# Kernel tuning notes

Measured on AMD Instinct MI355X. Metric: run time of the kernel, lower is better.

Reference implementation:

```python
import jax, jax.numpy as jnp
import numpy as np

T, B, D = 200, 1024, 128
T_OBS = 140
L = 20       # rec_dims: encoder latent per mean/std
LAT = 32     # latents: generative latent dim
GRU_U = 200  # gru_units
UNITS = 100  # hidden units of ODE-func / z0 nets


def _lin(key, fan_in, fan_out):
    return jax.random.normal(key, (fan_in, fan_out), jnp.float32) / jnp.sqrt(jnp.float32(fan_in))


def setup_inputs() -> dict:
    key = jax.random.key(0)
    ks = jax.random.split(key, 20)
    gin = 2 * L + 2 * D  # GRU input: (mean,std) + (data,mask)
    inp = {
        "truth": jax.random.normal(ks[0], (T, B, D), jnp.float32),
        "t": jnp.arange(T, dtype=jnp.float32),
        "obs_idx": jnp.sort(jax.random.randint(ks[1], (T_OBS,), 0, T)),
        "eps": jax.random.normal(ks[2], (B, LAT), jnp.float32),
        # encoder ODE func (rec_layers=1 hidden layer of UNITS)
        "enc_w1": _lin(ks[3], L, UNITS), "enc_b1": jnp.zeros(UNITS, jnp.float32),
        "enc_w2": _lin(ks[4], UNITS, L), "enc_b2": jnp.zeros(L, jnp.float32),
        # GRU unit: update / reset / new-state nets
        "gru_uw1": _lin(ks[5], gin, GRU_U), "gru_ub1": jnp.zeros(GRU_U, jnp.float32),
        "gru_uw2": _lin(ks[6], GRU_U, 2 * L), "gru_ub2": jnp.zeros(2 * L, jnp.float32),
        "gru_rw1": _lin(ks[7], gin, GRU_U), "gru_rb1": jnp.zeros(GRU_U, jnp.float32),
        "gru_rw2": _lin(ks[8], GRU_U, 2 * L), "gru_rb2": jnp.zeros(2 * L, jnp.float32),
        "gru_nw1": _lin(ks[9], gin, GRU_U), "gru_nb1": jnp.zeros(GRU_U, jnp.float32),
        "gru_nw2": _lin(ks[10], GRU_U, 2 * L), "gru_nb2": jnp.zeros(2 * L, jnp.float32),
        # transform hidden -> z0 (mean,std)
        "z0_w1": _lin(ks[11], 2 * L, UNITS), "z0_b1": jnp.zeros(UNITS, jnp.float32),
        "z0_w2": _lin(ks[12], UNITS, 2 * LAT), "z0_b2": jnp.zeros(2 * LAT, jnp.float32),
        # decoder ODE func (gen_layers=2 hidden layers of UNITS)
        "dec_w1": _lin(ks[13], LAT, UNITS), "dec_b1": jnp.zeros(UNITS, jnp.float32),
        "dec_w2": _lin(ks[14], UNITS, UNITS), "dec_b2": jnp.zeros(UNITS, jnp.float32),
        "dec_w3": _lin(ks[15], UNITS, LAT), "dec_b3": jnp.zeros(LAT, jnp.float32),
        # readout latent -> data space
        "out_w": _lin(ks[16], LAT, D), "out_b": jnp.zeros(D, jnp.float32),
    }
    return inp


def _rk4(f, y, dt):
    k1 = f(y)
    k2 = f(y + 0.5 * dt * k1)
    k3 = f(y + 0.5 * dt * k2)
    k4 = f(y + dt * k3)
    return y + (dt / 6.0) * (k1 + 2.0 * k2 + 2.0 * k3 + k4)


def reference(truth, t, obs_idx, eps,
              enc_w1, enc_b1, enc_w2, enc_b2,
              gru_uw1, gru_ub1, gru_uw2, gru_ub2,
              gru_rw1, gru_rb1, gru_rw2, gru_rb2,
              gru_nw1, gru_nb1, gru_nw2, gru_nb2,
              z0_w1, z0_b1, z0_w2, z0_b2,
              dec_w1, dec_b1, dec_w2, dec_b2, dec_w3, dec_b3,
              out_w, out_b):
    enc_f = lambda y: jnp.tanh(y @ enc_w1 + enc_b1) @ enc_w2 + enc_b2
    dec_f = lambda z: (jnp.tanh(jnp.tanh(z @ dec_w1 + dec_b1) @ dec_w2 + dec_b2)
                       @ dec_w3 + dec_b3)

    # ----- ODE-RNN encoder, run_backwards=True over observed timesteps -----
    x_obs = truth[obs_idx][::-1]                     # [To, B, D], time-reversed
    t_obs = t[obs_idx][::-1]
    dts = jnp.concatenate([jnp.zeros(1, t.dtype), jnp.diff(t_obs)])  # <=0 steps

    def enc_step(carry, inp):
        ym, ys = carry                               # [B,L] each
        x, dt = inp
        ym = _rk4(enc_f, ym, dt)                     # evolve mean between obs
        xm = jnp.concatenate([x, jnp.ones_like(x)], -1)   # data + mask(=1)
        y = jnp.concatenate([ym, ys], -1)            # [B, 2L]
        yc = jnp.concatenate([y, xm], -1)            # [B, 2L+2D]
        u = jax.nn.sigmoid(jnp.tanh(yc @ gru_uw1 + gru_ub1) @ gru_uw2 + gru_ub2)
        r = jax.nn.sigmoid(jnp.tanh(yc @ gru_rw1 + gru_rb1) @ gru_rw2 + gru_rb2)
        nc = jnp.concatenate([y * r, xm], -1)
        ns = jnp.tanh(nc @ gru_nw1 + gru_nb1) @ gru_nw2 + gru_nb2
        nm, nsd = ns[:, :L], jnp.abs(ns[:, L:])
        new_y = (1.0 - u) * jnp.concatenate([nm, nsd], -1) + u * y
        return (new_y[:, :L], new_y[:, L:]), None

    nb = truth.shape[1]
    init = (jnp.zeros((nb, L), truth.dtype), jnp.zeros((nb, L), truth.dtype))
    (ym, ys), _ = jax.lax.scan(enc_step, init, (x_obs, dts))

    # ----- z0 posterior and sample (n_traj_samples=1) -----
    h = jnp.tanh(jnp.concatenate([ym, ys], -1) @ z0_w1 + z0_b1) @ z0_w2 + z0_b2
    z0_mean, z0_std = h[:, :LAT], jnp.abs(h[:, LAT:])
    z = z0_mean + eps * z0_std                       # [B, LAT]

    # ----- Neural ODE decoder over time_steps_to_predict = t -----
    def dec_step(zc, dt):
        zn = _rk4(dec_f, zc, dt)
        return zn, zn
    _, zs = jax.lax.scan(dec_step, z, jnp.diff(t))
    sol = jnp.concatenate([z[None], zs], 0)          # [T, B, LAT]

    out = sol @ out_w + out_b                        # [T, B, D]
    return jnp.transpose(out, (1, 0, 2))[None]       # [1, B, T, D]
```

## Files before the change

kernel.cpp:

```cpp
#include <hip/hip_runtime.h>
#include <math.h>

#define BB 1024
#define DD 128
#define NWG 256
#define CH 28
#define NCH 5

#define WS_WPACK 0
#define WS_B1E   81920
#define WS_W1Y   82560
#define WS_Y     106560
#define WS_Z     147520
#define WS_HPRE  180288
#define WS_SOL   180288

__global__ __launch_bounds__(256) void prep_kernel(
    const float* __restrict__ uw1, const float* __restrict__ ub1,
    const float* __restrict__ rw1, const float* __restrict__ rb1,
    const float* __restrict__ nw1, const float* __restrict__ nb1,
    float* __restrict__ ws)
{
    int tid = blockIdx.x * blockDim.x + threadIdx.x;
    int nth = gridDim.x * blockDim.x;
    for (int idx = tid; idx < 128 * 640; idx += nth) {
        int k = idx / 640, j = idx - k * 640;
        float v = 0.f;
        if (j < 600) {
            int g = j / 200, jj = j - g * 200;
            const float* w1 = (g == 0) ? uw1 : (g == 1) ? rw1 : nw1;
            v = w1[(40 + k) * 200 + jj];
        }
        ws[WS_WPACK + idx] = v;
    }
    for (int j = tid; j < 640; j += nth) {
        float s = 0.f;
        if (j < 600) {
            int g = j / 200, jj = j - g * 200;
            const float* w1 = (g == 0) ? uw1 : (g == 1) ? rw1 : nw1;
            const float* b1 = (g == 0) ? ub1 : (g == 1) ? rb1 : nb1;
            s = b1[jj];
            for (int k = 168; k < 296; ++k) s += w1[k * 200 + jj];
        }
        ws[WS_B1E + j] = s;
    }
    for (int idx = tid; idx < 40 * 600; idx += nth) {
        int k = idx / 600, j = idx - k * 600;
        int g = j / 200, jj = j - g * 200;
        const float* w1 = (g == 0) ? uw1 : (g == 1) ? rw1 : nw1;
        ws[WS_W1Y + idx] = w1[k * 200 + jj];
    }
}

__global__ __launch_bounds__(256) void hpre_gemm(
    const float* __restrict__ truth, const int* __restrict__ obs_idx,
    const float* __restrict__ ws, float* __restrict__ hpre, int s0)
{
    __shared__ float sx[64][68];
    __shared__ float sw[64][132];
    const int t0 = threadIdx.x;
    const int jt = blockIdx.x % 5;
    const int bt = (blockIdx.x / 5) % 16;
    const int sl = blockIdx.x / 80;
    const int oi = obs_idx[139 - (s0 + sl)];
    const int b0 = bt * 64;
    const float* wpack = ws + WS_WPACK;
    const float* b1e   = ws + WS_B1E;

    const int jj  = t0 & 15;
    const int bb4 = t0 >> 4;
    float acc[8][4];
#pragma unroll
    for (int m = 0; m < 8; ++m)
#pragma unroll
        for (int q = 0; q < 4; ++q) acc[m][q] = 0.f;

    for (int kh = 0; kh < 2; ++kh) {
        __syncthreads();
        for (int i = t0; i < 64 * 16; i += 256) {
            int bb = i >> 4, kq = i & 15;
            const float4 v = *(const float4*)&truth[((size_t)oi * BB + b0 + bb) * DD + kh * 64 + kq * 4];
            *(float4*)&sx[bb][kq * 4] = v;
        }
        for (int i = t0; i < 64 * 32; i += 256) {
            int kk = i >> 5, jq = i & 31;
            const float4 v = *(const float4*)&wpack[(kh * 64 + kk) * 640 + jt * 128 + jq * 4];
            *(float4*)&sw[kk][jq * 4] = v;
        }
        __syncthreads();
#pragma unroll 4
        for (int k = 0; k < 64; ++k) {
            float xv[4], wv[8];
#pragma unroll
            for (int q = 0; q < 4; ++q) xv[q] = sx[bb4 * 4 + q][k];
#pragma unroll
            for (int m = 0; m < 8; ++m) wv[m] = sw[k][jj + 16 * m];
#pragma unroll
            for (int m = 0; m < 8; ++m)
#pragma unroll
                for (int q = 0; q < 4; ++q) acc[m][q] += wv[m] * xv[q];
        }
    }
    const int bblk = bt * 16 + bb4;
#pragma unroll
    for (int m = 0; m < 8; ++m) {
        int j = jt * 128 + jj + 16 * m;
        if (j < 600) {
            float be = b1e[j];
#pragma unroll
            for (int q = 0; q < 4; ++q)
                hpre[(size_t)((sl * 256 + bblk) * 4 + q) * 600 + j] = acc[m][q] + be;
        }
    }
}

__global__ __launch_bounds__(256, 1) void enc_chunk(
    const float* __restrict__ tg, const int* __restrict__ obs_idx,
    const float* __restrict__ eps,
    const float* __restrict__ ew1, const float* __restrict__ eb1,
    const float* __restrict__ ew2, const float* __restrict__ eb2,
    const float* __restrict__ uw2, const float* __restrict__ ub2,
    const float* __restrict__ rw2, const float* __restrict__ rb2,
    const float* __restrict__ nw2, const float* __restrict__ nb2,
    const float* __restrict__ z0w1, const float* __restrict__ z0b1,
    const float* __restrict__ z0w2, const float* __restrict__ z0b2,
    float* __restrict__ ws, int s0)
{
    __shared__ float s_t[200];
    __shared__ int   s_oi[140];
    __shared__ __align__(16) float s_y[40][4];
    __shared__ __align__(16) float s_ytmp[20][4];
    __shared__ float s_kacc[20][4];
    __shared__ __align__(16) float s_hid[4][104];
    __shared__ float s_pe[20][4][2];
    __shared__ __align__(16) float s_ew1t[100 * 20];
    __shared__ __align__(16) float s_w2n[40 * 212];
    __shared__ __align__(16) float s_hur[4][416];
    __shared__ __align__(16) float s_hn[4][208];
    __shared__ float s_pw[80][4][4];
    __shared__ float s_pn[40][4][4];
    __shared__ float s_u[40][4];
    __shared__ __align__(16) float s_yr[40][4];
    __shared__ float s_z0o[4][64];

    const int t0 = threadIdx.x;
    const int bblk = blockIdx.x;
    const int b0 = bblk * 4;
    const float* hpre = ws + WS_HPRE;

    float rgy[3][40];
    float rew2h[52];
    float rw2q[2][52];
    float eb1_r = 0.f, eb2_r = 0.f, bur_r = 0.f, bn_r = 0.f;

    if (t0 < 200) {
#pragma unroll
        for (int g = 0; g < 3; ++g)
#pragma unroll
            for (int k = 0; k < 40; ++k)
                rgy[g][k] = ws[WS_W1Y + k * 600 + g * 200 + t0];
    }
    if (t0 < 100) eb1_r = eb1[t0];
    if (t0 < 160) {
        const int c2 = t0 % 20, kh = t0 / 80;
#pragma unroll
        for (int i = 0; i < 52; ++i) {
            const int row = kh * 52 + i;
            rew2h[i] = (row < 100) ? ew2[row * 20 + c2] : 0.f;
        }
    }
    if (t0 < 80) eb2_r = eb2[t0 % 20];
    if (t0 < 160) {
        const int p = t0 % 20, g = (t0 / 20) % 2, kq = t0 / 40;
        const float* w2 = g ? rw2 : uw2;
#pragma unroll
        for (int j = 0; j < 2; ++j)
#pragma unroll
            for (int i = 0; i < 52; ++i) {
                const int row = kq * 52 + i;
                rw2q[j][i] = (row < 200) ? w2[row * 40 + p + 20 * j] : 0.f;
            }
        bur_r = ((t0 % 80) < 40) ? ub2[t0 % 80] : rb2[(t0 % 80) - 40];
        bn_r = nb2[t0 % 40];
    }

    for (int i = t0; i < 2000; i += 256) { int k = i / 100, c = i % 100; s_ew1t[c * 20 + k] = ew1[i]; }
    for (int i = t0; i < 40 * 212; i += 256) { int o = i / 212, k = i % 212; s_w2n[i] = (k < 200) ? nw2[k * 40 + o] : 0.f; }
    for (int i = t0; i < 200; i += 256) s_t[i] = tg[i];
    for (int i = t0; i < 140; i += 256) s_oi[i] = obs_idx[i];
    if (t0 < 160) { int k = t0 % 40, b = t0 / 40; s_y[k][b] = s0 ? ws[WS_Y + k * 1024 + b0 + b] : 0.f; }
    if (t0 < 4) {
#pragma unroll
        for (int i = 0; i < 4; ++i) s_hid[t0][100 + i] = 0.f;
#pragma unroll
        for (int i = 0; i < 8; ++i) { s_hur[t0][200 + i] = 0.f; s_hur[t0][408 + i] = 0.f; s_hn[t0][200 + i] = 0.f; }
    }
    __syncthreads();

    for (int sl = 0; sl < CH; ++sl) {
        const int s = s0 + sl;
        const int oi = s_oi[139 - s];
        const float dt = (s == 0) ? 0.f : (s_t[oi] - s_t[s_oi[140 - s]]);

        float hpu[4], hpr[4], hpn[4];
        if (t0 < 200) {
#pragma unroll
            for (int q = 0; q < 4; ++q) {
                const size_t r = (size_t)((sl * 256 + bblk) * 4 + q) * 600;
                hpu[q] = hpre[r + t0];
                hpr[q] = hpre[r + 200 + t0];
                hpn[q] = hpre[r + 400 + t0];
            }
        }

#pragma unroll 1
        for (int e = 0; e < 4; ++e) {
            if (t0 < 100) {
                const int c = t0;
                float a[4] = {eb1_r, eb1_r, eb1_r, eb1_r};
#pragma unroll
                for (int i = 0; i < 5; ++i) {
                    const float4 wv = *(const float4*)&s_ew1t[c * 20 + 4 * i];
                    const float wk[4] = {wv.x, wv.y, wv.z, wv.w};
#pragma unroll
                    for (int kk = 0; kk < 4; ++kk) {
                        const int k = 4 * i + kk;
                        const float4 yv = (e == 0) ? *(const float4*)&s_y[k][0]
                                                   : *(const float4*)&s_ytmp[k][0];
                        a[0] += wk[kk] * yv.x; a[1] += wk[kk] * yv.y;
                        a[2] += wk[kk] * yv.z; a[3] += wk[kk] * yv.w;
                    }
                }
#pragma unroll
                for (int b = 0; b < 4; ++b) s_hid[b][c] = tanhf(a[b]);
            }
            __syncthreads();
            if (t0 < 160) {
                const int c2 = t0 % 20, b = (t0 / 20) % 4, kh = t0 / 80;
                float acc = 0.f;
#pragma unroll
                for (int i = 0; i < 13; ++i) {
                    const float4 hv = *(const float4*)&s_hid[b][kh * 52 + 4 * i];
                    acc += hv.x * rew2h[4 * i] + hv.y * rew2h[4 * i + 1]
                         + hv.z * rew2h[4 * i + 2] + hv.w * rew2h[4 * i + 3];
                }
                s_pe[c2][b][kh] = acc;
            }
            __syncthreads();
            if (t0 < 80) {
                const int c2 = t0 % 20, b = t0 / 20;
                const float kv = eb2_r + s_pe[c2][b][0] + s_pe[c2][b][1];
                const float y0 = s_y[c2][b];
                if (e == 0)      { s_kacc[c2][b] = kv;        s_ytmp[c2][b] = y0 + 0.5f * dt * kv; }
                else if (e == 1) { s_kacc[c2][b] += 2.f * kv; s_ytmp[c2][b] = y0 + 0.5f * dt * kv; }
                else if (e == 2) { s_kacc[c2][b] += 2.f * kv; s_ytmp[c2][b] = y0 + dt * kv; }
                else             { s_y[c2][b] = y0 + (dt / 6.f) * (s_kacc[c2][b] + kv); }
            }
            __syncthreads();
        }

        if (t0 < 200) {
            float au[4], ar[4];
#pragma unroll
            for (int b = 0; b < 4; ++b) { au[b] = hpu[b]; ar[b] = hpr[b]; }
#pragma unroll
            for (int k = 0; k < 40; ++k) {
                const float4 yv = *(const float4*)&s_y[k][0];
                const float wu = rgy[0][k], wr = rgy[1][k];
                au[0] += wu * yv.x; au[1] += wu * yv.y; au[2] += wu * yv.z; au[3] += wu * yv.w;
                ar[0] += wr * yv.x; ar[1] += wr * yv.y; ar[2] += wr * yv.z; ar[3] += wr * yv.w;
            }
#pragma unroll
            for (int b = 0; b < 4; ++b) {
                s_hur[b][t0] = tanhf(au[b]);
                s_hur[b][208 + t0] = tanhf(ar[b]);
            }
        }
        __syncthreads();

        if (t0 < 160) {
            const int p = t0 % 20, g = (t0 / 20) % 2, kq = t0 / 40;
            const int goff = g * 208;
            float a1[4] = {0.f, 0.f, 0.f, 0.f}, a2[4] = {0.f, 0.f, 0.f, 0.f};
#pragma unroll
            for (int i = 0; i < 13; ++i) {
                const float wa = rw2q[0][4 * i], wb = rw2q[0][4 * i + 1],
                            wc = rw2q[0][4 * i + 2], wd = rw2q[0][4 * i + 3];
                const float we = rw2q[1][4 * i], wf = rw2q[1][4 * i + 1],
                            wg = rw2q[1][4 * i + 2], wh = rw2q[1][4 * i + 3];
#pragma unroll
                for (int b = 0; b < 4; ++b) {
                    const float4 hv = *(const float4*)&s_hur[b][goff + kq * 52 + 4 * i];
                    a1[b] += hv.x * wa + hv.y * wb + hv.z * wc + hv.w * wd;
                    a2[b] += hv.x * we + hv.y * wf + hv.z * wg + hv.w * wh;
                }
            }
            const int o1 = 40 * g + p, o2 = o1 + 20;
#pragma unroll
            for (int b = 0; b < 4; ++b) { s_pw[o1][b][kq] = a1[b]; s_pw[o2][b][kq] = a2[b]; }
        }
        __syncthreads();

        if (t0 < 160) {
            const int o = t0 % 80, bp = t0 / 80;
#pragma unroll
            for (int j = 0; j < 2; ++j) {
                const int b = 2 * bp + j;
                const float v = bur_r + s_pw[o][b][0] + s_pw[o][b][1] + s_pw[o][b][2] + s_pw[o][b][3];
                const float sg = 1.f / (1.f + expf(-v));
                if (o < 40) s_u[o][b] = sg;
                else        s_yr[o - 40][b] = s_y[o - 40][b] * sg;
            }
        }
        __syncthreads();

        if (t0 < 200) {
            float an[4];
#pragma unroll
            for (int b = 0; b < 4; ++b) an[b] = hpn[b];
#pragma unroll
            for (int k = 0; k < 40; ++k) {
                const float4 yv = *(const float4*)&s_yr[k][0];
                const float w = rgy[2][k];
                an[0] += w * yv.x; an[1] += w * yv.y; an[2] += w * yv.z; an[3] += w * yv.w;
            }
#pragma unroll
            for (int b = 0; b < 4; ++b) s_hn[b][t0] = tanhf(an[b]);
        }
        __syncthreads();

        if (t0 < 160) {
            const int o = t0 % 40, kq = t0 / 40;
            float an[4] = {0.f, 0.f, 0.f, 0.f};
#pragma unroll
            for (int i = 0; i < 13; ++i) {
                const float4 wv = *(const float4*)&s_w2n[o * 212 + kq * 52 + 4 * i];
#pragma unroll
                for (int b = 0; b < 4; ++b) {
                    const float4 hv = *(const float4*)&s_hn[b][kq * 52 + 4 * i];
                    an[b] += hv.x * wv.x + hv.y * wv.y + hv.z * wv.z + hv.w * wv.w;
                }
            }
#pragma unroll
            for (int b = 0; b < 4; ++b) s_pn[o][b][kq] = an[b];
        }
        __syncthreads();

        if (t0 < 160) {
            const int o = t0 % 40, b = t0 / 40;
            const float v = bn_r + s_pn[o][b][0] + s_pn[o][b][1] + s_pn[o][b][2] + s_pn[o][b][3];
            const float cand = (o < 20) ? v : fabsf(v);
            const float uu = s_u[o][b];
            s_y[o][b] = (1.f - uu) * cand + uu * s_y[o][b];
        }
        __syncthreads();
    }

    if (s0 + CH == 140) {
        if (t0 < 100) {
            const int c = t0;
            float a[4] = {z0b1[c], z0b1[c], z0b1[c], z0b1[c]};
#pragma unroll
            for (int k = 0; k < 40; ++k) {
                const float4 yv = *(const float4*)&s_y[k][0];
                const float w = z0w1[k * 100 + c];
                a[0] += w * yv.x; a[1] += w * yv.y; a[2] += w * yv.z; a[3] += w * yv.w;
            }
#pragma unroll
            for (int b = 0; b < 4; ++b) s_hid[b][c] = tanhf(a[b]);
        }
        __syncthreads();
        {
            const int b = t0 / 64, u = t0 % 64;
            float acc = z0b2[u];
#pragma unroll
            for (int i = 0; i < 25; ++i) {
                const float4 hv = *(const float4*)&s_hid[b][4 * i];
                acc += hv.x * z0w2[(4 * i) * 64 + u] + hv.y * z0w2[(4 * i + 1) * 64 + u]
                     + hv.z * z0w2[(4 * i + 2) * 64 + u] + hv.w * z0w2[(4 * i + 3) * 64 + u];
            }
            s_z0o[b][u] = acc;
        }
        __syncthreads();
        if (t0 < 128) {
            const int b = t0 / 32, i = t0 % 32;
            const int gb = b0 + b;
            ws[WS_Z + gb * 32 + i] = s_z0o[b][i] + eps[gb * 32 + i] * fabsf(s_z0o[b][32 + i]);
        }
    }
    if (t0 < 160) {
        const int k = t0 % 40, b = t0 / 40;
        ws[WS_Y + k * 1024 + b0 + b] = s_y[k][b];
    }
}

__global__ __launch_bounds__(256, 2) void dec_kernel(
    const float* __restrict__ tg,
    const float* __restrict__ dw1, const float* __restrict__ db1,
    const float* __restrict__ dw2, const float* __restrict__ db2,
    const float* __restrict__ dw3, const float* __restrict__ db3,
    float* __restrict__ ws)
{
    __shared__ float s_t[200];
    __shared__ __align__(16) float s_zt[2][32];
    __shared__ __align__(16) float s_h1[2][104];
    __shared__ __align__(16) float s_h2[2][104];

    const int t0 = threadIdx.x;
    const int b0 = blockIdx.x * 2;

    const bool isA = (t0 < 200);
    const bool isB = (t0 >= 224);
    const int cA = isA ? (t0 % 100) : 0;
    const int bA = isA ? (t0 / 100) : 0;
    const int c3 = isB ? (t0 - 224) : 0;

    float rw[132];
    float bias1 = 0.f, bias2 = 0.f;
    float z_r[2] = {0.f, 0.f}, ka_r[2] = {0.f, 0.f};

    if (isA) {
#pragma unroll
        for (int k = 0; k < 32; ++k)  rw[k] = dw1[k * 100 + cA];
#pragma unroll
        for (int k = 0; k < 100; ++k) rw[32 + k] = dw2[k * 100 + cA];
        bias1 = db1[cA]; bias2 = db2[cA];
    } else if (isB) {
#pragma unroll
        for (int k = 0; k < 100; ++k) rw[k] = dw3[k * 32 + c3];
#pragma unroll
        for (int k = 100; k < 132; ++k) rw[k] = 0.f;
        bias1 = db3[c3];
        z_r[0] = ws[WS_Z + (size_t)(b0 + 0) * 32 + c3];
        z_r[1] = ws[WS_Z + (size_t)(b0 + 1) * 32 + c3];
    } else {
#pragma unroll
        for (int k = 0; k < 132; ++k) rw[k] = 0.f;
    }
    for (int i = t0; i < 200; i += 256) s_t[i] = tg[i];
    if (t0 < 8) { s_h1[t0 >> 2][100 + (t0 & 3)] = 0.f; s_h2[t0 >> 2][100 + (t0 & 3)] = 0.f; }
    __syncthreads();

    for (int s = 0; s < 200; ++s) {
        if (isB) {
#pragma unroll
            for (int b = 0; b < 2; ++b) {
                ws[WS_SOL + (size_t)(s * 1024 + b0 + b) * 32 + c3] = z_r[b];
                s_zt[b][c3] = z_r[b];
            }
        }
        if (s == 199) break;
        const float dtv = s_t[s + 1] - s_t[s];
        __syncthreads();

#pragma unroll 1
        for (int e = 0; e < 4; ++e) {
            if (isA) {
                float a = bias1;
#pragma unroll
                for (int i = 0; i < 8; ++i) {
                    const float4 zv = *(const float4*)&s_zt[bA][4 * i];
                    a += zv.x * rw[4 * i] + zv.y * rw[4 * i + 1]
                       + zv.z * rw[4 * i + 2] + zv.w * rw[4 * i + 3];
                }
                s_h1[bA][cA] = tanhf(a);
            }
            __syncthreads();
            if (isA) {
                float a = bias2;
#pragma unroll
                for (int i = 0; i < 25; ++i) {
                    const float4 hv = *(const float4*)&s_h1[bA][4 * i];
                    a += hv.x * rw[32 + 4 * i] + hv.y * rw[32 + 4 * i + 1]
                       + hv.z * rw[32 + 4 * i + 2] + hv.w * rw[32 + 4 * i + 3];
                }
                s_h2[bA][cA] = tanhf(a);
            }
            __syncthreads();
            if (isB) {
#pragma unroll
                for (int b = 0; b < 2; ++b) {
                    float acc = bias1;
#pragma unroll
                    for (int i = 0; i < 25; ++i) {
                        const float4 hv = *(const float4*)&s_h2[b][4 * i];
                        acc += hv.x * rw[4 * i] + hv.y * rw[4 * i + 1]
                             + hv.z * rw[4 * i + 2] + hv.w * rw[4 * i + 3];
                    }
                    if (e == 0)      { ka_r[b] = acc;        s_zt[b][c3] = z_r[b] + 0.5f * dtv * acc; }
                    else if (e == 1) { ka_r[b] += 2.f * acc; s_zt[b][c3] = z_r[b] + 0.5f * dtv * acc; }
                    else if (e == 2) { ka_r[b] += 2.f * acc; s_zt[b][c3] = z_r[b] + dtv * acc; }
                    else             { z_r[b] += (dtv / 6.f) * (ka_r[b] + acc); }
                }
            }
            __syncthreads();
        }
    }
}

__global__ __launch_bounds__(256) void proj_kernel(
    const float* __restrict__ ow, const float* __restrict__ ob,
    const float* __restrict__ ws, float* __restrict__ out)
{
    const int t0 = threadIdx.x;
    const int d = t0 & 127, half = t0 >> 7;
    float rw[32];
#pragma unroll
    for (int k = 0; k < 32; ++k) rw[k] = ow[k * 128 + d];
    const float bo = ob[d];
    const int sb0 = blockIdx.x * 64 + half * 32;
#pragma unroll 2
    for (int m = 0; m < 32; ++m) {
        const int sb = sb0 + m;
        const int s = sb >> 10, b = sb & 1023;
        const float4* zp = (const float4*)&ws[WS_SOL + (size_t)sb * 32];
        float acc = bo;
#pragma unroll
        for (int kq = 0; kq < 8; ++kq) {
            const float4 zv = zp[kq];
            acc += zv.x * rw[4 * kq] + zv.y * rw[4 * kq + 1]
                 + zv.z * rw[4 * kq + 2] + zv.w * rw[4 * kq + 3];
        }
        out[((size_t)b * 200 + s) * 128 + d] = acc;
    }
}

extern "C" void kernel_launch(void* const* d_in, const int* in_sizes, int n_in,
                              void* d_out, int out_size, void* d_ws, size_t ws_size,
                              hipStream_t stream)
{
    const float* truth = (const float*)d_in[0];
    const float* tg    = (const float*)d_in[1];
    const int*   oi    = (const int*)d_in[2];
    const float* eps   = (const float*)d_in[3];
    const float* ew1   = (const float*)d_in[4];
    const float* eb1   = (const float*)d_in[5];
    const float* ew2   = (const float*)d_in[6];
    const float* eb2   = (const float*)d_in[7];
    const float* uw1   = (const float*)d_in[8];
    const float* ub1   = (const float*)d_in[9];
    const float* uw2   = (const float*)d_in[10];
    const float* ub2   = (const float*)d_in[11];
    const float* rw1   = (const float*)d_in[12];
    const float* rb1   = (const float*)d_in[13];
    const float* rw2   = (const float*)d_in[14];
    const float* rb2   = (const float*)d_in[15];
    const float* nw1   = (const float*)d_in[16];
    const float* nb1   = (const float*)d_in[17];
    const float* nw2   = (const float*)d_in[18];
    const float* nb2   = (const float*)d_in[19];
    const float* z0w1  = (const float*)d_in[20];
    const float* z0b1  = (const float*)d_in[21];
    const float* z0w2  = (const float*)d_in[22];
    const float* z0b2  = (const float*)d_in[23];
    const float* dw1   = (const float*)d_in[24];
    const float* db1   = (const float*)d_in[25];
    const float* dw2   = (const float*)d_in[26];
    const float* db2   = (const float*)d_in[27];
    const float* dw3   = (const float*)d_in[28];
    const float* db3   = (const float*)d_in[29];
    const float* ow    = (const float*)d_in[30];
    const float* ob    = (const float*)d_in[31];
    float* ws  = (float*)d_ws;
    float* out = (float*)d_out;

    prep_kernel<<<dim3(120), dim3(256), 0, stream>>>(uw1, ub1, rw1, rb1, nw1, nb1, ws);
    for (int c = 0; c < NCH; ++c) {
        hpre_gemm<<<dim3(CH * 16 * 5), dim3(256), 0, stream>>>(truth, oi, ws, ws + WS_HPRE, c * CH);
        enc_chunk<<<dim3(NWG), dim3(256), 0, stream>>>(
            tg, oi, eps, ew1, eb1, ew2, eb2, uw2, ub2, rw2, rb2, nw2, nb2,
            z0w1, z0b1, z0w2, z0b2, ws, c * CH);
    }
    dec_kernel<<<dim3(512), dim3(256), 0, stream>>>(tg, dw1, db1, dw2, db2, dw3, db3, ws);
    proj_kernel<<<dim3(3200), dim3(256), 0, stream>>>(ow, ob, ws, out);
}
```

Measured before the change: 4.693 ms.

## Restructure decoder ODE to one wavefront per batch row with LDS weights

The decoder kernel now assigns one 64-lane wavefront to each batch element (4 per block, 256 blocks), keeping all three MLP weight matrices transposed in shared memory instead of per-thread registers. Because each wavefront owns its own batch row, the block-wide barriers between RK4 stages are removed and the work relies on intra-wavefront lockstep execution plus a lane shuffle for the final reduction. This cuts synchronisation and idle lanes, but the weights are now read from LDS on every stage rather than from registers, and correctness depends on wavefront-synchronous shared-memory visibility with no explicit fence.

```diff
diff --git a/kernel.cpp b/kernel.cpp
--- a/kernel.cpp
+++ b/kernel.cpp
@@ -394,106 +394,111 @@
     }
 }
 
-__global__ __launch_bounds__(256, 2) void dec_kernel(
+__global__ __launch_bounds__(256, 1) void dec_kernel(
     const float* __restrict__ tg,
     const float* __restrict__ dw1, const float* __restrict__ db1,
     const float* __restrict__ dw2, const float* __restrict__ db2,
     const float* __restrict__ dw3, const float* __restrict__ db3,
     float* __restrict__ ws)
 {
+    __shared__ __align__(16) float s_w1t[100][36];
+    __shared__ __align__(16) float s_w2t[100][100];
+    __shared__ __align__(16) float s_w3t[32][108];
+    __shared__ float s_b1[100], s_b2[100], s_b3[32];
     __shared__ float s_t[200];
-    __shared__ __align__(16) float s_zt[2][32];
-    __shared__ __align__(16) float s_h1[2][104];
-    __shared__ __align__(16) float s_h2[2][104];
+    __shared__ __align__(16) float s_zt[4][32];
+    __shared__ __align__(16) float s_h1[4][104];
+    __shared__ __align__(16) float s_h2[4][104];
 
     const int t0 = threadIdx.x;
-    const int b0 = blockIdx.x * 2;
-
-    const bool isA = (t0 < 200);
-    const bool isB = (t0 >= 224);
-    const int cA = isA ? (t0 % 100) : 0;
-    const int bA = isA ? (t0 / 100) : 0;
-    const int c3 = isB ? (t0 - 224) : 0;
-
-    float rw[132];
-    float bias1 = 0.f, bias2 = 0.f;
-    float z_r[2] = {0.f, 0.f}, ka_r[2] = {0.f, 0.f};
-
-    if (isA) {
-#pragma unroll
-        for (int k = 0; k < 32; ++k)  rw[k] = dw1[k * 100 + cA];
-#pragma unroll
-        for (int k = 0; k < 100; ++k) rw[32 + k] = dw2[k * 100 + cA];
-        bias1 = db1[cA]; bias2 = db2[cA];
-    } else if (isB) {
-#pragma unroll
-        for (int k = 0; k < 100; ++k) rw[k] = dw3[k * 32 + c3];
-#pragma unroll
-        for (int k = 100; k < 132; ++k) rw[k] = 0.f;
-        bias1 = db3[c3];
-        z_r[0] = ws[WS_Z + (size_t)(b0 + 0) * 32 + c3];
-        z_r[1] = ws[WS_Z + (size_t)(b0 + 1) * 32 + c3];
-    } else {
-#pragma unroll
-        for (int k = 0; k < 132; ++k) rw[k] = 0.f;
+    const int w  = t0 >> 6;
+    const int l  = t0 & 63;
+    const int batch = blockIdx.x * 4 + w;
+
+    for (int i = t0; i < 3200; i += 256)  { int k = i / 100, c = i - k * 100; s_w1t[c][k] = dw1[i]; }
+    for (int i = t0; i < 10000; i += 256) { int k = i / 100, c = i - k * 100; s_w2t[c][k] = dw2[i]; }
+    for (int i = t0; i < 3200; i += 256)  { int k = i >> 5,  j = i & 31;      s_w3t[j][k] = dw3[i]; }
+    if (t0 < 100) { s_b1[t0] = db1[t0]; s_b2[t0] = db2[t0]; }
+    if (t0 < 32) {
+        s_b3[t0] = db3[t0];
+#pragma unroll
+        for (int i = 100; i < 108; ++i) s_w3t[t0][i] = 0.f;
     }
     for (int i = t0; i < 200; i += 256) s_t[i] = tg[i];
-    if (t0 < 8) { s_h1[t0 >> 2][100 + (t0 & 3)] = 0.f; s_h2[t0 >> 2][100 + (t0 & 3)] = 0.f; }
+    if (t0 < 16) s_h2[t0 >> 2][100 + (t0 & 3)] = 0.f;
+
+    float z_r = 0.f, ka_r = 0.f;
+    if (l < 32) z_r = ws[WS_Z + (size_t)batch * 32 + l];
     __syncthreads();
+    if (l < 32) s_zt[w][l] = z_r;
+
+    const int c0 = l;
+    const int c1 = 64 + l;
+    const int j3   = l & 31;
+    const int koff = (l >> 5) * 52;
 
     for (int s = 0; s < 200; ++s) {
-        if (isB) {
-#pragma unroll
-            for (int b = 0; b < 2; ++b) {
-                ws[WS_SOL + (size_t)(s * 1024 + b0 + b) * 32 + c3] = z_r[b];
-                s_zt[b][c3] = z_r[b];
-            }
-        }
+        if (l < 32)
+            ws[WS_SOL + (size_t)(s * 1024 + batch) * 32 + l] = z_r;
         if (s == 199) break;
         const float dtv = s_t[s + 1] - s_t[s];
-        __syncthreads();
 
 #pragma unroll 1
         for (int e = 0; e < 4; ++e) {
-            if (isA) {
-                float a = bias1;
+            float4 zv[8];
+#pragma unroll
+            for (int i = 0; i < 8; ++i) zv[i] = *(const float4*)&s_zt[w][4 * i];
+            {
+                float a0 = s_b1[c0];
 #pragma unroll
                 for (int i = 0; i < 8; ++i) {
-                    const float4 zv = *(const float4*)&s_zt[bA][4 * i];
-                    a += zv.x * rw[4 * i] + zv.y * rw[4 * i + 1]
-                       + zv.z * rw[4 * i + 2] + zv.w * rw[4 * i + 3];
-                }
-                s_h1[bA][cA] = tanhf(a);
-            }
-            __syncthreads();
-            if (isA) {
-                float a = bias2;
+                    const float4 wv = *(const float4*)&s_w1t[c0][4 * i];
+                    a0 += zv[i].x * wv.x + zv[i].y * wv.y + zv[i].z * wv.z + zv[i].w * wv.w;
+                }
+                s_h1[w][c0] = tanhf(a0);
+            }
+            if (l < 36) {
+                float a1 = s_b1[c1];
+#pragma unroll
+                for (int i = 0; i < 8; ++i) {
+                    const float4 wv = *(const float4*)&s_w1t[c1][4 * i];
+                    a1 += zv[i].x * wv.x + zv[i].y * wv.y + zv[i].z * wv.z + zv[i].w * wv.w;
+                }
+                s_h1[w][c1] = tanhf(a1);
+            }
+            {
+                float a0 = s_b2[c0];
 #pragma unroll
                 for (int i = 0; i < 25; ++i) {
-                    const float4 hv = *(const float4*)&s_h1[bA][4 * i];
-                    a += hv.x * rw[32 + 4 * i] + hv.y * rw[32 + 4 * i + 1]
-                       + hv.z * rw[32 + 4 * i + 2] + hv.w * rw[32 + 4 * i + 3];
-                }
-                s_h2[bA][cA] = tanhf(a);
-            }
-            __syncthreads();
-            if (isB) {
-#pragma unroll
-                for (int b = 0; b < 2; ++b) {
-                    float acc = bias1;
-#pragma unroll
-                    for (int i = 0; i < 25; ++i) {
-                        const float4 hv = *(const float4*)&s_h2[b][4 * i];
-                        acc += hv.x * rw[4 * i] + hv.y * rw[4 * i + 1]
-                             + hv.z * rw[4 * i + 2] + hv.w * rw[4 * i + 3];
-                    }
-                    if (e == 0)      { ka_r[b] = acc;        s_zt[b][c3] = z_r[b] + 0.5f * dtv * acc; }
-                    else if (e == 1) { ka_r[b] += 2.f * acc; s_zt[b][c3] = z_r[b] + 0.5f * dtv * acc; }
-                    else if (e == 2) { ka_r[b] += 2.f * acc; s_zt[b][c3] = z_r[b] + dtv * acc; }
-                    else             { z_r[b] += (dtv / 6.f) * (ka_r[b] + acc); }
-                }
-            }
-            __syncthreads();
+                    const float4 hv = *(const float4*)&s_h1[w][4 * i];
+                    const float4 wv = *(const float4*)&s_w2t[c0][4 * i];
+                    a0 += hv.x * wv.x + hv.y * wv.y + hv.z * wv.z + hv.w * wv.w;
+                }
+                s_h2[w][c0] = tanhf(a0);
+            }
+            if (l < 36) {
+                float a1 = s_b2[c1];
+#pragma unroll
+                for (int i = 0; i < 25; ++i) {
+                    const float4 hv = *(const float4*)&s_h1[w][4 * i];
+                    const float4 wv = *(const float4*)&s_w2t[c1][4 * i];
+                    a1 += hv.x * wv.x + hv.y * wv.y + hv.z * wv.z + hv.w * wv.w;
+                }
+                s_h2[w][c1] = tanhf(a1);
+            }
+            float acc = 0.f;
+#pragma unroll
+            for (int i = 0; i < 13; ++i) {
+                const float4 hv = *(const float4*)&s_h2[w][koff + 4 * i];
+                const float4 wv = *(const float4*)&s_w3t[j3][koff + 4 * i];
+                acc += hv.x * wv.x + hv.y * wv.y + hv.z * wv.z + hv.w * wv.w;
+            }
+            acc += __shfl_xor(acc, 32);
+            const float kj = acc + s_b3[j3];
+            if (e == 0)      { ka_r = kj;          if (l < 32) s_zt[w][l] = z_r + 0.5f * dtv * kj; }
+            else if (e == 1) { ka_r += 2.f * kj;   if (l < 32) s_zt[w][l] = z_r + 0.5f * dtv * kj; }
+            else if (e == 2) { ka_r += 2.f * kj;   if (l < 32) s_zt[w][l] = z_r + dtv * kj; }
+            else             { z_r += (dtv / 6.f) * (ka_r + kj); if (l < 32) s_zt[w][l] = z_r; }
         }
     }
 }
@@ -571,6 +576,6 @@
             tg, oi, eps, ew1, eb1, ew2, eb2, uw2, ub2, rw2, rb2, nw2, nb2,
             z0w1, z0b1, z0w2, z0b2, ws, c * CH);
     }
-    dec_kernel<<<dim3(512), dim3(256), 0, stream>>>(tg, dw1, db1, dw2, db2, dw3, db3, ws);
+    dec_kernel<<<dim3(256), dim3(256), 0, stream>>>(tg, dw1, db1, dw2, db2, dw3, db3, ws);
     proj_kernel<<<dim3(3200), dim3(256), 0, stream>>>(ow, ob, ws, out);
 }
```

Measured after the change: 4.813 ms. +2.6%, slower.

## Split decoder ODE MLP over K across waves with readlane broadcasts and fast tanh

Applied to the files above, without the earlier changes.

Rewrites the decoder RK4 kernel so that each of the four wavefronts owns a slice of the reduction dimension. Activations are broadcast through readlane instead of shared-memory float4 reads, and per-wave partial sums are reduced through shared memory. Every thread redundantly keeps the full z state, which removes one barrier per step and idle thread groups. It also swaps tanhf/expf for exp2/rcp-based approximations across the encoder and decoder, trading some accuracy for fewer instructions.

```diff
diff --git a/kernel.cpp b/kernel.cpp
--- a/kernel.cpp
+++ b/kernel.cpp
@@ -14,6 +14,19 @@
 #define WS_Z     147520
 #define WS_HPRE  180288
 #define WS_SOL   180288
+
+__device__ __forceinline__ float bcast(float v, int lane) {
+    return __uint_as_float(__builtin_amdgcn_readlane(__float_as_uint(v), lane));
+}
+
+__device__ __forceinline__ float tanh_fast(float x) {
+    const float t = __builtin_amdgcn_exp2f(x * 2.88539008177793f);
+    return 1.f - 2.f * __builtin_amdgcn_rcpf(t + 1.f);
+}
+__device__ __forceinline__ float sigm_fast(float x) {
+    const float t = __builtin_amdgcn_exp2f(x * -1.4426950408889634f);
+    return __builtin_amdgcn_rcpf(1.f + t);
+}
 
 __global__ __launch_bounds__(256) void prep_kernel(
     const float* __restrict__ uw1, const float* __restrict__ ub1,
@@ -232,7 +245,7 @@
                     }
                 }
 #pragma unroll
-                for (int b = 0; b < 4; ++b) s_hid[b][c] = tanhf(a[b]);
+                for (int b = 0; b < 4; ++b) s_hid[b][c] = tanh_fast(a[b]);
             }
             __syncthreads();
             if (t0 < 160) {
@@ -272,8 +285,8 @@
             }
 #pragma unroll
             for (int b = 0; b < 4; ++b) {
-                s_hur[b][t0] = tanhf(au[b]);
-                s_hur[b][208 + t0] = tanhf(ar[b]);
+                s_hur[b][t0] = tanh_fast(au[b]);
+                s_hur[b][208 + t0] = tanh_fast(ar[b]);
             }
         }
         __syncthreads();
@@ -307,7 +320,7 @@
             for (int j = 0; j < 2; ++j) {
                 const int b = 2 * bp + j;
                 const float v = bur_r + s_pw[o][b][0] + s_pw[o][b][1] + s_pw[o][b][2] + s_pw[o][b][3];
-                const float sg = 1.f / (1.f + expf(-v));
+                const float sg = sigm_fast(v);
                 if (o < 40) s_u[o][b] = sg;
                 else        s_yr[o - 40][b] = s_y[o - 40][b] * sg;
             }
@@ -325,7 +338,7 @@
                 an[0] += w * yv.x; an[1] += w * yv.y; an[2] += w * yv.z; an[3] += w * yv.w;
             }
 #pragma unroll
-            for (int b = 0; b < 4; ++b) s_hn[b][t0] = tanhf(an[b]);
+            for (int b = 0; b < 4; ++b) s_hn[b][t0] = tanh_fast(an[b]);
         }
         __syncthreads();
 
@@ -367,7 +380,7 @@
                 a[0] += w * yv.x; a[1] += w * yv.y; a[2] += w * yv.z; a[3] += w * yv.w;
             }
 #pragma unroll
-            for (int b = 0; b < 4; ++b) s_hid[b][c] = tanhf(a[b]);
+            for (int b = 0; b < 4; ++b) s_hid[b][c] = tanh_fast(a[b]);
         }
         __syncthreads();
         {
@@ -402,98 +415,133 @@
     float* __restrict__ ws)
 {
     __shared__ float s_t[200];
-    __shared__ __align__(16) float s_zt[2][32];
-    __shared__ __align__(16) float s_h1[2][104];
-    __shared__ __align__(16) float s_h2[2][104];
+    __shared__ float s_p1[4][2][144];
+    __shared__ float s_p2[4][2][144];
+    __shared__ float s_p3[4][2][32];
 
     const int t0 = threadIdx.x;
+    const int w  = t0 >> 6;
+    const int l  = t0 & 63;
+    const int wu = __builtin_amdgcn_readfirstlane(w);
     const int b0 = blockIdx.x * 2;
 
-    const bool isA = (t0 < 200);
-    const bool isB = (t0 >= 224);
-    const int cA = isA ? (t0 % 100) : 0;
-    const int bA = isA ? (t0 / 100) : 0;
-    const int c3 = isB ? (t0 - 224) : 0;
-
-    float rw[132];
-    float bias1 = 0.f, bias2 = 0.f;
-    float z_r[2] = {0.f, 0.f}, ka_r[2] = {0.f, 0.f};
-
-    if (isA) {
-#pragma unroll
-        for (int k = 0; k < 32; ++k)  rw[k] = dw1[k * 100 + cA];
-#pragma unroll
-        for (int k = 0; k < 100; ++k) rw[32 + k] = dw2[k * 100 + cA];
-        bias1 = db1[cA]; bias2 = db2[cA];
-    } else if (isB) {
-#pragma unroll
-        for (int k = 0; k < 100; ++k) rw[k] = dw3[k * 32 + c3];
-#pragma unroll
-        for (int k = 100; k < 132; ++k) rw[k] = 0.f;
-        bias1 = db3[c3];
-        z_r[0] = ws[WS_Z + (size_t)(b0 + 0) * 32 + c3];
-        z_r[1] = ws[WS_Z + (size_t)(b0 + 1) * 32 + c3];
-    } else {
-#pragma unroll
-        for (int k = 0; k < 132; ++k) rw[k] = 0.f;
-    }
+    const int c0 = l;
+    const int c1 = 64 + l;
+    const bool has1 = (l < 36);
+    const int j3 = l & 31;
+    const int r2 = 25 * w;
+
+    float rw1a[8], rw1b[8], rw2a[25], rw2b[25], rw3[25];
+#pragma unroll
+    for (int i = 0; i < 8; ++i) {
+        rw1a[i] = dw1[(8 * w + i) * 100 + c0];
+        rw1b[i] = has1 ? dw1[(8 * w + i) * 100 + c1] : 0.f;
+    }
+#pragma unroll
+    for (int i = 0; i < 25; ++i) {
+        rw2a[i] = dw2[(r2 + i) * 100 + c0];
+        rw2b[i] = has1 ? dw2[(r2 + i) * 100 + c1] : 0.f;
+        rw3[i]  = dw3[(r2 + i) * 32 + j3];
+    }
+    float b1s = 0.f, b2s = 0.f;
+    if (l < 25) { b1s = db1[r2 + l]; b2s = db2[r2 + l]; }
+    const float b3d = db3[j3];
+
     for (int i = t0; i < 200; i += 256) s_t[i] = tg[i];
-    if (t0 < 8) { s_h1[t0 >> 2][100 + (t0 & 3)] = 0.f; s_h2[t0 >> 2][100 + (t0 & 3)] = 0.f; }
+
+    float z0d = ws[WS_Z + (size_t)(b0 + 0) * 32 + j3];
+    float z1d = ws[WS_Z + (size_t)(b0 + 1) * 32 + j3];
+    float ka0 = 0.f, ka1 = 0.f;
+    float zs0 = z0d, zs1 = z1d;
     __syncthreads();
 
     for (int s = 0; s < 200; ++s) {
-        if (isB) {
-#pragma unroll
-            for (int b = 0; b < 2; ++b) {
-                ws[WS_SOL + (size_t)(s * 1024 + b0 + b) * 32 + c3] = z_r[b];
-                s_zt[b][c3] = z_r[b];
-            }
-        }
+        if (t0 < 64)
+            ws[WS_SOL + (size_t)(s * 1024 + b0 + (t0 >> 5)) * 32 + (t0 & 31)]
+                = (t0 < 32) ? z0d : z1d;
         if (s == 199) break;
         const float dtv = s_t[s + 1] - s_t[s];
-        __syncthreads();
 
 #pragma unroll 1
         for (int e = 0; e < 4; ++e) {
-            if (isA) {
-                float a = bias1;
+            {
+                float a00 = 0.f, a01 = 0.f, a10 = 0.f, a11 = 0.f;
+                const int zb = 8 * wu;
 #pragma unroll
                 for (int i = 0; i < 8; ++i) {
-                    const float4 zv = *(const float4*)&s_zt[bA][4 * i];
-                    a += zv.x * rw[4 * i] + zv.y * rw[4 * i + 1]
-                       + zv.z * rw[4 * i + 2] + zv.w * rw[4 * i + 3];
-                }
-                s_h1[bA][cA] = tanhf(a);
+                    const float sv0 = bcast(zs0, zb + i);
+                    const float sv1 = bcast(zs1, zb + i);
+                    a00 += sv0 * rw1a[i]; a01 += sv1 * rw1a[i];
+                    a10 += sv0 * rw1b[i]; a11 += sv1 * rw1b[i];
+                }
+                s_p1[w][0][c0] = a00; s_p1[w][1][c0] = a01;
+                if (has1) { s_p1[w][0][c1] = a10; s_p1[w][1][c1] = a11; }
             }
             __syncthreads();
-            if (isA) {
-                float a = bias2;
+
+            float h10, h11;
+            {
+                const int rc = r2 + l;
+                const float v0 = s_p1[0][0][rc] + s_p1[1][0][rc] + s_p1[2][0][rc] + s_p1[3][0][rc];
+                const float v1 = s_p1[0][1][rc] + s_p1[1][1][rc] + s_p1[2][1][rc] + s_p1[3][1][rc];
+                h10 = tanh_fast(b1s + v0);
+                h11 = tanh_fast(b1s + v1);
+            }
+
+            {
+                float a00 = 0.f, a01 = 0.f, a10 = 0.f, a11 = 0.f;
 #pragma unroll
                 for (int i = 0; i < 25; ++i) {
-                    const float4 hv = *(const float4*)&s_h1[bA][4 * i];
-                    a += hv.x * rw[32 + 4 * i] + hv.y * rw[32 + 4 * i + 1]
-                       + hv.z * rw[32 + 4 * i + 2] + hv.w * rw[32 + 4 * i + 3];
-                }
-                s_h2[bA][cA] = tanhf(a);
+                    const float sv0 = bcast(h10, i);
+                    const float sv1 = bcast(h11, i);
+                    a00 += sv0 * rw2a[i]; a01 += sv1 * rw2a[i];
+                    a10 += sv0 * rw2b[i]; a11 += sv1 * rw2b[i];
+                }
+                s_p2[w][0][c0] = a00; s_p2[w][1][c0] = a01;
+                if (has1) { s_p2[w][0][c1] = a10; s_p2[w][1][c1] = a11; }
             }
             __syncthreads();
-            if (isB) {
-#pragma unroll
-                for (int b = 0; b < 2; ++b) {
-                    float acc = bias1;
-#pragma unroll
-                    for (int i = 0; i < 25; ++i) {
-                        const float4 hv = *(const float4*)&s_h2[b][4 * i];
-                        acc += hv.x * rw[4 * i] + hv.y * rw[4 * i + 1]
-                             + hv.z * rw[4 * i + 2] + hv.w * rw[4 * i + 3];
-                    }
-                    if (e == 0)      { ka_r[b] = acc;        s_zt[b][c3] = z_r[b] + 0.5f * dtv * acc; }
-                    else if (e == 1) { ka_r[b] += 2.f * acc; s_zt[b][c3] = z_r[b] + 0.5f * dtv * acc; }
-                    else if (e == 2) { ka_r[b] += 2.f * acc; s_zt[b][c3] = z_r[b] + dtv * acc; }
-                    else             { z_r[b] += (dtv / 6.f) * (ka_r[b] + acc); }
-                }
+
+            float h20, h21;
+            {
+                const int rc = r2 + l;
+                const float v0 = s_p2[0][0][rc] + s_p2[1][0][rc] + s_p2[2][0][rc] + s_p2[3][0][rc];
+                const float v1 = s_p2[0][1][rc] + s_p2[1][1][rc] + s_p2[2][1][rc] + s_p2[3][1][rc];
+                h20 = tanh_fast(b2s + v0);
+                h21 = tanh_fast(b2s + v1);
+            }
+
+            {
+                float ap0 = 0.f, ap1 = 0.f;
+#pragma unroll
+                for (int i = 0; i < 25; ++i) {
+                    ap0 += bcast(h20, i) * rw3[i];
+                    ap1 += bcast(h21, i) * rw3[i];
+                }
+                if (l < 32) { s_p3[w][0][l] = ap0; s_p3[w][1][l] = ap1; }
             }
             __syncthreads();
+
+            {
+                const float kj0 = b3d + s_p3[0][0][j3] + s_p3[1][0][j3]
+                                      + s_p3[2][0][j3] + s_p3[3][0][j3];
+                const float kj1 = b3d + s_p3[0][1][j3] + s_p3[1][1][j3]
+                                      + s_p3[2][1][j3] + s_p3[3][1][j3];
+                if (e == 0) {
+                    ka0 = kj0; ka1 = kj1;
+                    zs0 = z0d + 0.5f * dtv * kj0; zs1 = z1d + 0.5f * dtv * kj1;
+                } else if (e == 1) {
+                    ka0 += 2.f * kj0; ka1 += 2.f * kj1;
+                    zs0 = z0d + 0.5f * dtv * kj0; zs1 = z1d + 0.5f * dtv * kj1;
+                } else if (e == 2) {
+                    ka0 += 2.f * kj0; ka1 += 2.f * kj1;
+                    zs0 = z0d + dtv * kj0; zs1 = z1d + dtv * kj1;
+                } else {
+                    z0d += (dtv / 6.f) * (ka0 + kj0);
+                    z1d += (dtv / 6.f) * (ka1 + kj1);
+                    zs0 = z0d; zs1 = z1d;
+                }
+            }
         }
     }
 }
```

New measurement: 4.013 ms. -14.5%, faster.
